# Kernel optimization log

Hardware: AMD Instinct MI355X
Metric: run time of the kernel (lower is better)

The kernel has to match this reference:

```python
import jax, jax.numpy as jnp
import numpy as np

L = 16          # num transformer layers
D = 1024        # d_model
H = 16          # num heads
HD = 64         # head dim
LDIM = 512      # latent dim
TC = 512        # text conditioning length
PAST = 1024     # kv cache past length
FF = 4096       # ffn hidden
FH = 2048       # flow net hidden
MAX_PERIOD = 10000.0


def _ln(x, w, b, eps=1e-5):
    mu = jnp.mean(x, axis=-1, keepdims=True)
    var = jnp.mean((x - mu) ** 2, axis=-1, keepdims=True)
    return (x - mu) * jax.lax.rsqrt(var + eps) * w + b


def setup_inputs() -> dict:
    key = jax.random.key(0)
    ks = jax.random.split(key, 13)
    n = lambda k, s: jax.random.normal(k, s, dtype=jnp.float32)
    inp = {
        'text_embeddings': n(ks[0], (1, TC, D)),
        'prev_latent': n(ks[1], (1, 1, LDIM)),
        'kv_cache': n(ks[2], (L, 2, 1, PAST, H, HD)),
        'cache_len': PAST,
        'noise': n(ks[3], (1, LDIM)),
        'bos_emb': n(ks[4], (LDIM,)),
        'W_in': n(ks[5], (LDIM, D)) * 0.02, 'b_in': jnp.zeros((D,), jnp.float32),
        'ln1_w': jnp.ones((L, D), jnp.float32), 'ln1_b': jnp.zeros((L, D), jnp.float32),
        'Wqkv': n(ks[6], (L, D, 3 * D)) * 0.02, 'bqkv': jnp.zeros((L, 3 * D), jnp.float32),
        'Wo': n(ks[7], (L, D, D)) * 0.02, 'bo': jnp.zeros((L, D), jnp.float32),
        'ln2_w': jnp.ones((L, D), jnp.float32), 'ln2_b': jnp.zeros((L, D), jnp.float32),
        'W1': n(ks[8], (L, D, FF)) * 0.02, 'b1': jnp.zeros((L, FF), jnp.float32),
        'W2': n(ks[9], (L, FF, D)) * 0.02, 'b2': jnp.zeros((L, D), jnp.float32),
        'on_w': jnp.ones((D,), jnp.float32), 'on_b': jnp.zeros((D,), jnp.float32),
        'W_eos': n(ks[10], (D, 1)) * 0.02, 'b_eos': jnp.zeros((1,), jnp.float32),
        'Wf1': n(ks[11], (D + 2 + LDIM, FH)) * 0.02, 'bf1': jnp.zeros((FH,), jnp.float32),
        'Wf2': n(ks[12], (FH, LDIM)) * 0.02, 'bf2': jnp.zeros((LDIM,), jnp.float32),
    }
    return inp


def reference(text_embeddings, prev_latent, kv_cache, cache_len, noise, bos_emb,
              W_in, b_in, ln1_w, ln1_b, Wqkv, bqkv, Wo, bo, ln2_w, ln2_b,
              W1, b1, W2, b2, on_w, on_b, W_eos, b_eos, Wf1, bf1, Wf2, bf2):
    B = prev_latent.shape[0]
    prev = jnp.where(jnp.isnan(prev_latent), bos_emb[None, None, :], prev_latent)
    x = jnp.concatenate([text_embeddings, prev @ W_in + b_in], axis=1)  # [B,T,D]
    T = x.shape[1]
    Tkv = kv_cache.shape[3] + T

    # RoPE angles, shared across layers (offset = cache_len)
    half = HD // 2
    freqs = jnp.exp(jnp.arange(half, dtype=jnp.float32) * (-np.log(MAX_PERIOD) * 2.0 / HD))
    ts = jnp.arange(T, dtype=jnp.float32) + jnp.asarray(cache_len, jnp.float32)
    ang = ts[:, None] * freqs[None, :]               # [T, half]
    cos = jnp.cos(ang)[None, :, None, :]             # [1,T,1,half]
    sin = jnp.sin(ang)[None, :, None, :]

    # causal mask: new token q can see all past + itself
    mask = jnp.arange(Tkv)[None, :] <= (Tkv - T + jnp.arange(T)[:, None])  # [T,Tkv]
    scale = 1.0 / np.sqrt(HD)

    def rot(t):
        tr = t.reshape(B, T, H, half, 2)
        r, i = tr[..., 0], tr[..., 1]
        return jnp.stack([r * cos - i * sin, r * sin + i * cos], axis=-1).reshape(B, T, H, HD)

    def layer_fn(xc, p):
        l1w, l1b, wqkv, bq, wo, bo_, l2w, l2b, w1, b1_, w2, b2_, kv = p
        h = _ln(xc, l1w, l1b)
        qkv = (h @ wqkv + bq).reshape(B, T, 3, H, HD)
        q, k, v = qkv[:, :, 0], qkv[:, :, 1], qkv[:, :, 2]
        q, k = rot(q), rot(k)
        q = q.transpose(0, 2, 1, 3)                  # [B,H,T,HD]
        k = k.transpose(0, 2, 1, 3)
        v = v.transpose(0, 2, 1, 3)
        pk = kv[0].transpose(0, 2, 1, 3)             # [B,H,past,HD]
        pv = kv[1].transpose(0, 2, 1, 3)
        fk = jnp.concatenate([pk, k], axis=2)        # [B,H,Tkv,HD]
        fv = jnp.concatenate([pv, v], axis=2)
        scores = jnp.einsum('bhqd,bhkd->bhqk', q, fk) * scale
        scores = jnp.where(mask[None, None], scores, -1e30)
        attn = jax.nn.softmax(scores, axis=-1)
        o = jnp.einsum('bhqk,bhkd->bhqd', attn, fv).transpose(0, 2, 1, 3).reshape(B, T, D)
        xc = xc + o @ wo + bo_
        h2 = _ln(xc, l2w, l2b)
        xc = xc + jax.nn.gelu(h2 @ w1 + b1_, approximate=False) @ w2 + b2_
        new_kv = jnp.stack([fk.transpose(0, 2, 1, 3), fv.transpose(0, 2, 1, 3)])
        return xc, new_kv

    xs = (ln1_w, ln1_b, Wqkv, bqkv, Wo, bo, ln2_w, ln2_b, W1, b1, W2, b2, kv_cache)
    x, new_kv_cache = jax.lax.scan(layer_fn, x, xs)

    x = _ln(x.astype(jnp.float32), on_w, on_b)
    t_out = x[:, -1, :]                              # [B,D]
    is_eos = (t_out @ W_eos + b_eos) > -4.0
    s_time = jnp.zeros((B, 1), noise.dtype)
    t_time = jnp.ones((B, 1), noise.dtype)
    f_in = jnp.concatenate([t_out, s_time, t_time, noise], axis=-1)
    flow_dir = jax.nn.gelu(f_in @ Wf1 + bf1, approximate=False) @ Wf2 + bf2
    next_latent = noise + flow_dir
    new_cache_len = cache_len + T
    return next_latent, is_eos, new_kv_cache, new_cache_len
```

## Files before the change

kernel.cpp:

```cpp
#include <hip/hip_runtime.h>
#include <math.h>

#define KV_LS_STRIDE 1573888
#define KV_OUT_OFF 513
#define CLEN_OUT_IDX 50364929
#define VTP 1600
#define KVL 1638400

typedef __attribute__((ext_vector_type(8))) short short8;
typedef __attribute__((ext_vector_type(4))) short short4v;
typedef __attribute__((ext_vector_type(4))) float f32x4;

static __device__ __forceinline__ float gelu_f(float v){
  return 0.5f * v * (1.0f + erff(v * 0.70710678118654752f));
}
static __device__ __forceinline__ unsigned short f2b(float f){
  unsigned int u = __float_as_uint(f);
  u += 0x7fffu + ((u>>16)&1u);
  return (unsigned short)(u>>16);
}
__device__ __forceinline__ void gload16(const void* g, void* l){
  __builtin_amdgcn_global_load_lds((const __attribute__((address_space(1))) void*)g,
                                   (__attribute__((address_space(3))) void*)l, 16, 0, 0);
}

__global__ __launch_bounds__(256) void copy_text_k(const float4* __restrict__ t,
                                                   float4* __restrict__ x){
  int i = blockIdx.x*256 + threadIdx.x;
  x[i] = t[i];
}

__global__ __launch_bounds__(256) void build512_k(const float* __restrict__ prev,
    const float* __restrict__ bos, const float* __restrict__ Win,
    const float* __restrict__ bin, float* __restrict__ x){
  __shared__ float red[16][17];
  int t = threadIdx.x;
  int n = blockIdx.x*16 + (t&15), ks = t>>4;
  float s = 0.f;
  for (int k=ks*32; k<ks*32+32; ++k){
    float p = prev[k];
    if (p != p) p = bos[k];
    s += p * Win[(size_t)k*1024 + n];
  }
  red[ks][t&15] = s;
  __syncthreads();
  if (t < 16){
    float acc = bin[blockIdx.x*16 + t];
    #pragma unroll
    for (int j=0;j<16;++j) acc += red[j][t];
    x[(size_t)512*1024 + blockIdx.x*16 + t] = acc;
  }
}

__global__ __launch_bounds__(256) void rope_tab_k(float* __restrict__ cost,
    float* __restrict__ sint, const int* __restrict__ clen){
  int i = blockIdx.x*256 + threadIdx.x;
  if (i >= 513*32) return;
  int t = i >> 5, j = i & 31;
  float freq = expf((float)j * (-0.28782313662425572f));
  float ang = (float)(t + clen[0]) * freq;
  cost[i] = cosf(ang);
  sint[i] = sinf(ang);
}

template<int BF16OUT>
__global__ __launch_bounds__(256) void ln_k(const float* __restrict__ x,
    const float* __restrict__ w, const float* __restrict__ b,
    float* __restrict__ outf, unsigned short* __restrict__ outh, int rows){
  int row = blockIdx.x; if (row >= rows) return;
  const float* xr = x + (size_t)row*1024;
  int tid = threadIdx.x;
  float4 v = *(const float4*)(xr + tid*4);
  float s  = v.x+v.y+v.z+v.w;
  float ss = v.x*v.x+v.y*v.y+v.z*v.z+v.w*v.w;
  for (int o=32;o;o>>=1){ s += __shfl_down(s,o); ss += __shfl_down(ss,o); }
  __shared__ float red[8];
  int wid = tid>>6;
  if ((tid&63)==0){ red[wid]=s; red[4+wid]=ss; }
  __syncthreads();
  if (tid==0){
    float ts = red[0]+red[1]+red[2]+red[3];
    float tss= red[4]+red[5]+red[6]+red[7];
    float mu = ts*(1.0f/1024.0f);
    float var= tss*(1.0f/1024.0f) - mu*mu;
    red[0]=mu; red[1]=rsqrtf(var + 1e-5f);
  }
  __syncthreads();
  float mu = red[0], rs = red[1];
  float4 wv = *(const float4*)(w + tid*4);
  float4 bv = *(const float4*)(b + tid*4);
  float4 o4;
  o4.x = (v.x-mu)*rs*wv.x + bv.x;
  o4.y = (v.y-mu)*rs*wv.y + bv.y;
  o4.z = (v.z-mu)*rs*wv.z + bv.z;
  o4.w = (v.w-mu)*rs*wv.w + bv.w;
  if (BF16OUT){
    uint2 u;
    u.x = (unsigned)f2b(o4.x) | ((unsigned)f2b(o4.y)<<16);
    u.y = (unsigned)f2b(o4.z) | ((unsigned)f2b(o4.w)<<16);
    *(uint2*)(outh + (size_t)row*1024 + tid*4) = u;
  } else {
    *(float4*)(outf + (size_t)row*1024 + tid*4) = o4;
  }
}

__global__ __launch_bounds__(256) void wtrans_k(const float* __restrict__ W,
    unsigned short* __restrict__ Wt, int K, int N){
  __shared__ float s[64][68];
  int l = blockIdx.z;
  W  += (size_t)l*K*N;
  Wt += (size_t)l*N*K;
  int t = threadIdx.x;
  int n0 = blockIdx.x*64, k0 = blockIdx.y*64;
  int r = t>>4, c4 = (t&15)<<2;
  #pragma unroll
  for (int p=0;p<4;++p){
    float4 v = *(const float4*)(W + (size_t)(k0 + r + p*16)*N + n0 + c4);
    *(float4*)&s[r + p*16][c4] = v;
  }
  __syncthreads();
  int n = t>>2, ks = t&3;
  unsigned short tmp[16];
  #pragma unroll
  for (int j=0;j<16;++j) tmp[j] = f2b(s[ks*16 + j][n]);
  size_t ob = (size_t)(n0+n)*K + k0 + ks*16;
  uint4 lo, hi;
  lo.x = tmp[0] | ((unsigned)tmp[1]<<16);  lo.y = tmp[2] | ((unsigned)tmp[3]<<16);
  lo.z = tmp[4] | ((unsigned)tmp[5]<<16);  lo.w = tmp[6] | ((unsigned)tmp[7]<<16);
  hi.x = tmp[8] | ((unsigned)tmp[9]<<16);  hi.y = tmp[10]| ((unsigned)tmp[11]<<16);
  hi.z = tmp[12]| ((unsigned)tmp[13]<<16); hi.w = tmp[14]| ((unsigned)tmp[15]<<16);
  *(uint4*)(Wt + ob)     = lo;
  *(uint4*)(Wt + ob + 8) = hi;
}

template<int MODE>
__global__ __launch_bounds__(256,4) void mgemm64_k(const unsigned short* __restrict__ A,
    const unsigned short* __restrict__ Bt, float* __restrict__ P,
    const float* __restrict__ bias, unsigned short* __restrict__ outh,
    int M, int N, int K, int kc,
    const float* __restrict__ cost, const float* __restrict__ sint,
    unsigned short* __restrict__ qb16, unsigned short* __restrict__ kb16,
    unsigned short* __restrict__ vt, float* __restrict__ kl, float* __restrict__ vl){
  __shared__ unsigned short Alds[2][64*64];
  __shared__ unsigned short Blds[2][64*64];
  int tid = threadIdx.x;
  int w = tid>>6, l = tid&63;
  int m0 = blockIdx.y*64, n0 = blockIdx.x*64;
  int k0 = blockIdx.z*kc, k1 = k0+kc;
  f32x4 acc[2][2];
  #pragma unroll
  for (int i=0;i<2;++i)
    #pragma unroll
    for (int j=0;j<2;++j) acc[i][j] = (f32x4){0.f,0.f,0.f,0.f};
  int srow = l>>3;
  int scol = (((l&7) ^ (srow&7)))*8;
  const unsigned short* ga  = A  + (size_t)(m0 + w*16 + srow)*K + scol;
  const unsigned short* gbp = Bt + (size_t)(n0 + w*16 + srow)*K + scol;
  int lofs = w*16*64;
  int wr = w>>1, wc = w&1, lr = l&15, lg = l>>4;
  int sw = (lr&7)<<3;
  gload16(ga + k0,                &Alds[0][lofs]);
  gload16(ga + (size_t)8*K + k0,  &Alds[0][lofs + 512]);
  gload16(gbp + k0,               &Blds[0][lofs]);
  gload16(gbp + (size_t)8*K + k0, &Blds[0][lofs + 512]);
  __syncthreads();
  int cur = 0;
  for (int k=k0; k<k1; k+=64){
    if (k + 64 < k1){
      int nb = cur^1, kn = k + 64;
      gload16(ga + kn,                &Alds[nb][lofs]);
      gload16(ga + (size_t)8*K + kn,  &Alds[nb][lofs + 512]);
      gload16(gbp + kn,               &Blds[nb][lofs]);
      gload16(gbp + (size_t)8*K + kn, &Blds[nb][lofs + 512]);
    }
    const unsigned short* la = &Alds[cur][0];
    const unsigned short* lb = &Blds[cur][0];
    #pragma unroll
    for (int kk=0; kk<2; ++kk){
      short8 af[2], bfr[2];
      #pragma unroll
      for (int mi=0;mi<2;++mi)
        af[mi] = *(const short8*)&la[(wr*32 + mi*16 + lr)*64 + ((kk*32 + lg*8) ^ sw)];
      #pragma unroll
      for (int ni=0;ni<2;++ni)
        bfr[ni] = *(const short8*)&lb[(wc*32 + ni*16 + lr)*64 + ((kk*32 + lg*8) ^ sw)];
      #pragma unroll
      for (int mi=0;mi<2;++mi)
        #pragma unroll
        for (int ni=0;ni<2;++ni)
          acc[mi][ni] = __builtin_amdgcn_mfma_f32_16x16x32_bf16(af[mi], bfr[ni], acc[mi][ni], 0, 0, 0);
    }
    __syncthreads();
    cur ^= 1;
  }
  if constexpr (MODE==3){
    int nt = n0 >> 6;
    int kind = nt >> 4;
    int hh = nt & 15;
    #pragma unroll
    for (int mi=0;mi<2;++mi){
      int rb = m0 + wr*32 + mi*16 + lg*4;
      #pragma unroll
      for (int ni=0;ni<2;++ni){
        int d = wc*32 + ni*16 + lr;
        float bcol = bias[n0 + d];
        if (kind == 2){
          unsigned short pk[4];
          #pragma unroll
          for (int r=0;r<4;++r){
            float v = acc[mi][ni][r] + bcol;
            pk[r] = f2b(v);
            int t = rb + r;
            if (t < 513) vl[(size_t)(1024+t)*1024 + hh*64 + d] = v;
          }
          uint2 u2;
          u2.x = pk[0] | ((unsigned)pk[1]<<16);
          u2.y = pk[2] | ((unsigned)pk[3]<<16);
          *(uint2*)(vt + (size_t)(hh*64+d)*VTP + 1024 + rb) = u2;
        } else {
          int j = d >> 1;
          #pragma unroll
          for (int r=0;r<4;++r){
            float v = acc[mi][ni][r] + bcol;
            float p = __shfl_xor(v, 1);
            int t = rb + r;
            int tc = (t < 513) ? t : 0;
            float c = cost[(tc<<5)+j], s = sint[(tc<<5)+j];
            float o = (d&1) ? (p*s + v*c) : (v*c - p*s);
            if (t < 513){
              if (kind == 0){
                qb16[(size_t)t*1024 + hh*64 + d] = f2b(o*0.125f);
              } else {
                size_t ko = (size_t)(1024+t)*1024 + hh*64 + d;
                kb16[ko] = f2b(o);
                kl[ko] = o;
              }
            }
          }
        }
      }
    }
  } else {
    float* Pz = P + (size_t)blockIdx.z*M*N;
    #pragma unroll
    for (int mi=0;mi<2;++mi){
      int rb = m0 + wr*32 + mi*16 + lg*4;
      #pragma unroll
      for (int ni=0;ni<2;++ni){
        int col = n0 + wc*32 + ni*16 + lr;
        float bcol = (MODE!=0) ? bias[col] : 0.f;
        #pragma unroll
        for (int r=0;r<4;++r){
          int row = rb + r;
          if (row < M){
            if constexpr (MODE==0){
              Pz[(size_t)row*N + col] = acc[mi][ni][r];
            } else {
              outh[(size_t)row*N + col] = f2b(gelu_f(acc[mi][ni][r] + bcol));
            }
          }
        }
      }
    }
  }
}

template<int KS, int DOLN>
__global__ __launch_bounds__(256) void reduce_ln_k(const float* __restrict__ P,
    const float* __restrict__ bias, float* __restrict__ x,
    const float* __restrict__ lnw, const float* __restrict__ lnb,
    unsigned short* __restrict__ outh){
  const int M = 513;
  int row = blockIdx.x;
  int tid = threadIdx.x;
  int c4 = tid<<2;
  float4 sv = *(const float4*)(P + (size_t)row*1024 + c4);
  #pragma unroll
  for (int z=1; z<KS; ++z){
    float4 t = *(const float4*)(P + (size_t)z*M*1024 + (size_t)row*1024 + c4);
    sv.x+=t.x; sv.y+=t.y; sv.z+=t.z; sv.w+=t.w;
  }
  float4 bv = *(const float4*)(bias + c4);
  float4 xv = *(const float4*)(x + (size_t)row*1024 + c4);
  xv.x += sv.x+bv.x; xv.y += sv.y+bv.y; xv.z += sv.z+bv.z; xv.w += sv.w+bv.w;
  *(float4*)(x + (size_t)row*1024 + c4) = xv;
  if constexpr (DOLN){
    float s  = xv.x+xv.y+xv.z+xv.w;
    float ss = xv.x*xv.x+xv.y*xv.y+xv.z*xv.z+xv.w*xv.w;
    for (int o=32;o;o>>=1){ s += __shfl_down(s,o); ss += __shfl_down(ss,o); }
    __shared__ float red[8];
    int wid = tid>>6;
    if ((tid&63)==0){ red[wid]=s; red[4+wid]=ss; }
    __syncthreads();
    if (tid==0){
      float ts = red[0]+red[1]+red[2]+red[3];
      float tss= red[4]+red[5]+red[6]+red[7];
      float mu = ts*(1.0f/1024.0f);
      float var= tss*(1.0f/1024.0f) - mu*mu;
      red[0]=mu; red[1]=rsqrtf(var + 1e-5f);
    }
    __syncthreads();
    float mu = red[0], rs = red[1];
    float4 wv = *(const float4*)(lnw + c4);
    float4 bb = *(const float4*)(lnb + c4);
    float o0 = (xv.x-mu)*rs*wv.x + bb.x;
    float o1 = (xv.y-mu)*rs*wv.y + bb.y;
    float o2 = (xv.z-mu)*rs*wv.z + bb.z;
    float o3 = (xv.w-mu)*rs*wv.w + bb.w;
    uint2 u;
    u.x = (unsigned)f2b(o0) | ((unsigned)f2b(o1)<<16);
    u.y = (unsigned)f2b(o2) | ((unsigned)f2b(o3)<<16);
    *(uint2*)(outh + (size_t)row*1024 + c4) = u;
  }
}

__global__ __launch_bounds__(256) void past16_k(const float* __restrict__ kvin,
    unsigned short* __restrict__ kb, unsigned short* __restrict__ vt,
    float* __restrict__ kvout){
  __shared__ float s[64][68];
  int l = blockIdx.z;
  int hh = blockIdx.x, t0 = blockIdx.y*64;
  const float* kvK = kvin + (size_t)l*2097152;
  const float* kvV = kvK + 1048576;
  unsigned short* kbL = kb + (size_t)l*KVL;
  unsigned short* vtL = vt + (size_t)l*KVL;
  float* kl = kvout + (size_t)(2*l)  *KV_LS_STRIDE;
  float* vl = kvout + (size_t)(2*l+1)*KV_LS_STRIDE;
  int tid = threadIdx.x;
  int row = tid>>4, c4 = (tid&15)<<2;
  #pragma unroll
  for (int p=0;p<4;++p){
    int rr = row + p*16;
    size_t off = (size_t)(t0+rr)*1024 + hh*64 + c4;
    float4 v = *(const float4*)(kvK + off);
    uint2 u;
    u.x = (unsigned)f2b(v.x) | ((unsigned)f2b(v.y)<<16);
    u.y = (unsigned)f2b(v.z) | ((unsigned)f2b(v.w)<<16);
    *(uint2*)(kbL + off) = u;
    kl[off]=v.x; kl[off+1]=v.y; kl[off+2]=v.z; kl[off+3]=v.w;
    float4 w = *(const float4*)(kvV + off);
    *(float4*)&s[rr][c4] = w;
    vl[off]=w.x; vl[off+1]=w.y; vl[off+2]=w.z; vl[off+3]=w.w;
  }
  __syncthreads();
  int n = tid>>2, ks = tid&3;
  unsigned short tmp[16];
  #pragma unroll
  for (int j=0;j<16;++j) tmp[j] = f2b(s[ks*16+j][n]);
  size_t ob = (size_t)(hh*64+n)*VTP + t0 + ks*16;
  uint4 lo, hi;
  lo.x = tmp[0] | ((unsigned)tmp[1]<<16);  lo.y = tmp[2] | ((unsigned)tmp[3]<<16);
  lo.z = tmp[4] | ((unsigned)tmp[5]<<16);  lo.w = tmp[6] | ((unsigned)tmp[7]<<16);
  hi.x = tmp[8] | ((unsigned)tmp[9]<<16);  hi.y = tmp[10]| ((unsigned)tmp[11]<<16);
  hi.z = tmp[12]| ((unsigned)tmp[13]<<16); hi.w = tmp[14]| ((unsigned)tmp[15]<<16);
  *(uint4*)(vtL + ob)     = lo;
  *(uint4*)(vtL + ob + 8) = hi;
}

static __device__ __forceinline__ f32x4 mfma32(short8 a, short8 b, f32x4 c){
  return __builtin_amdgcn_mfma_f32_16x16x32_bf16(a, b, c, 0, 0, 0);
}

__global__ __launch_bounds__(128) void attn_k(const unsigned short* __restrict__ qb,
    const unsigned short* __restrict__ kb, const unsigned short* __restrict__ vt,
    float* __restrict__ Oc, float* __restrict__ ml){
  const int T=513, Tkv=1537, past=1024;
  int hh = blockIdx.x, bt = blockIdx.y, ch = blockIdx.z;
  int wv = threadIdx.x >> 6, l = threadIdx.x & 63;
  int g = l >> 4, lr = l & 15;
  int q0 = bt*32 + wv*16;
  int gq = q0 + lr;
  const unsigned short* qp = qb + (size_t)gq*1024 + hh*64 + g*8;
  short8 qf0 = *(const short8*)qp;
  short8 qf1 = *(const short8*)(qp+32);
  f32x4 acc_o[4];
  #pragma unroll
  for (int i=0;i<4;++i) acc_o[i] = (f32x4){0.f,0.f,0.f,0.f};
  float m_run = -1e30f, l_run = 0.f;
  int kend_w = past + q0 + 16; if (kend_w > Tkv) kend_w = Tkv;
  int kstart = ch*384;
  int kend = (ch==3) ? kend_w : ((ch+1)*384 < kend_w ? (ch+1)*384 : kend_w);
  for (int kt0 = kstart; kt0 < kend; kt0 += 64){
    float p[16];
    #pragma unroll
    for (int st=0; st<4; ++st){
      const unsigned short* kp = kb + (size_t)(kt0+st*16+lr)*1024 + hh*64 + g*8;
      short8 kf0 = *(const short8*)kp;
      short8 kf1 = *(const short8*)(kp+32);
      f32x4 s4 = (f32x4){0.f,0.f,0.f,0.f};
      s4 = mfma32(kf0, qf0, s4);
      s4 = mfma32(kf1, qf1, s4);
      #pragma unroll
      for (int r=0;r<4;++r) p[st*4+r] = s4[r];
    }
    if (kt0 + 63 > past + q0 + 15 || kt0 + 63 >= Tkv){
      #pragma unroll
      for (int st=0; st<4; ++st)
        #pragma unroll
        for (int r=0;r<4;++r){
          int kt = kt0 + st*16 + g*4 + r;
          if (kt > past + gq || kt >= Tkv) p[st*4+r] = -1e30f;
        }
    }
    float tmax = p[0];
    #pragma unroll
    for (int i=1;i<16;++i) tmax = fmaxf(tmax, p[i]);
    tmax = fmaxf(tmax, __shfl_xor(tmax,16));
    tmax = fmaxf(tmax, __shfl_xor(tmax,32));
    float m_new = fmaxf(m_run, tmax);
    float sc = __expf(m_run - m_new);
    float psum = 0.f;
    #pragma unroll
    for (int i=0;i<16;++i){ p[i] = __expf(p[i] - m_new); psum += p[i]; }
    psum += __shfl_xor(psum,16); psum += __shfl_xor(psum,32);
    l_run = l_run*sc + psum;
    m_run = m_new;
    #pragma unroll
    for (int db=0;db<4;++db){
      acc_o[db][0]*=sc; acc_o[db][1]*=sc; acc_o[db][2]*=sc; acc_o[db][3]*=sc;
    }
    short8 pf[2];
    #pragma unroll
    for (int sp=0; sp<2; ++sp){
      union { short8 s8; unsigned int u[4]; } pu;
      pu.u[0] = (unsigned)f2b(p[sp*8+0]) | ((unsigned)f2b(p[sp*8+1])<<16);
      pu.u[1] = (unsigned)f2b(p[sp*8+2]) | ((unsigned)f2b(p[sp*8+3])<<16);
      pu.u[2] = (unsigned)f2b(p[sp*8+4]) | ((unsigned)f2b(p[sp*8+5])<<16);
      pu.u[3] = (unsigned)f2b(p[sp*8+6]) | ((unsigned)f2b(p[sp*8+7])<<16);
      pf[sp] = pu.s8;
    }
    #pragma unroll
    for (int sp=0; sp<2; ++sp){
      #pragma unroll
      for (int db=0; db<4; ++db){
        const unsigned short* vp = vt + (size_t)(hh*64 + db*16 + lr)*VTP + kt0 + sp*32 + g*4;
        short4v va0 = *(const short4v*)vp;
        short4v va1 = *(const short4v*)(vp + 16);
        short8 va = (short8){va0[0],va0[1],va0[2],va0[3],va1[0],va1[1],va1[2],va1[3]};
        acc_o[db] = mfma32(va, pf[sp], acc_o[db]);
      }
    }
  }
  if (gq < T){
    size_t ob = ((size_t)(ch*16+hh)*544 + gq)*64;
    #pragma unroll
    for (int db=0;db<4;++db)
      *(float4*)(Oc + ob + db*16 + g*4) = make_float4(acc_o[db][0],acc_o[db][1],acc_o[db][2],acc_o[db][3]);
    if (g==0){
      size_t mo = ((size_t)(ch*16+hh)*544 + gq)*2;
      ml[mo] = m_run; ml[mo+1] = l_run;
    }
  }
}

__global__ __launch_bounds__(256) void attn_comb_k(const float* __restrict__ Oc,
    const float* __restrict__ ml, unsigned short* __restrict__ obb){
  int qg = blockIdx.x;
  int t = threadIdx.x;
  int hh = t>>4, d4 = (t&15)<<2;
  float m[4], lv[4];
  float mm = -1e30f;
  #pragma unroll
  for (int c=0;c<4;++c){
    size_t mo = ((size_t)(c*16+hh)*544 + qg)*2;
    m[c]=ml[mo]; lv[c]=ml[mo+1];
    mm = fmaxf(mm, m[c]);
  }
  float w[4], denom = 0.f;
  #pragma unroll
  for (int c=0;c<4;++c){ w[c] = __expf(m[c]-mm); denom += lv[c]*w[c]; }
  float inv = 1.0f/denom;
  float r0=0.f,r1=0.f,r2=0.f,r3=0.f;
  #pragma unroll
  for (int c=0;c<4;++c){
    float4 o = *(const float4*)(Oc + (((size_t)(c*16+hh)*544+qg)*64 + d4));
    r0 += o.x*w[c]; r1 += o.y*w[c]; r2 += o.z*w[c]; r3 += o.w*w[c];
  }
  r0*=inv; r1*=inv; r2*=inv; r3*=inv;
  uint2 u;
  u.x = (unsigned)f2b(r0) | ((unsigned)f2b(r1)<<16);
  u.y = (unsigned)f2b(r2) | ((unsigned)f2b(r3)<<16);
  *(uint2*)(obb + (size_t)qg*1024 + hh*64 + d4) = u;
}

__global__ __launch_bounds__(256) void eos_tail_k(const float* __restrict__ tout,
    const float* __restrict__ Weos, const float* __restrict__ beos,
    const int* __restrict__ clen, float* __restrict__ out){
  int tid = threadIdx.x;
  float s = 0.f;
  for (int i=tid;i<1024;i+=256) s += tout[i]*Weos[i];
  for (int o=32;o;o>>=1) s += __shfl_down(s,o);
  __shared__ float red[4];
  if ((tid&63)==0) red[tid>>6] = s;
  __syncthreads();
  if (tid==0){
    float v = red[0]+red[1]+red[2]+red[3] + beos[0];
    out[512] = (v > -4.0f) ? 1.0f : 0.0f;
    out[CLEN_OUT_IDX] = (float)(clen[0] + 513);
  }
}

__global__ __launch_bounds__(256) void flow1_k(const float* __restrict__ tout,
    const float* __restrict__ noise, const float* __restrict__ Wf1,
    const float* __restrict__ bf1, float* __restrict__ fh){
  __shared__ float red[16][17];
  int t = threadIdx.x;
  int n = blockIdx.x*16 + (t&15), ks = t>>4;
  float s = 0.f;
  for (int k=ks*96; k<ks*96+96; ++k){
    float in = (k < 1024) ? tout[k] : noise[k-1024];
    size_t krow = (k < 1024) ? (size_t)k : (size_t)(k+2);
    s += in * Wf1[krow*2048 + n];
  }
  red[ks][t&15] = s;
  __syncthreads();
  if (t < 16){
    int nn = blockIdx.x*16 + t;
    float acc = bf1[nn] + Wf1[(size_t)1025*2048 + nn];
    #pragma unroll
    for (int j=0;j<16;++j) acc += red[j][t];
    fh[nn] = gelu_f(acc);
  }
}

__global__ __launch_bounds__(256) void flow2_k(const float* __restrict__ fh,
    const float* __restrict__ noise, const float* __restrict__ Wf2,
    const float* __restrict__ bf2, float* __restrict__ out){
  __shared__ float red[16][17];
  int t = threadIdx.x;
  int n = blockIdx.x*16 + (t&15), ks = t>>4;
  float s = 0.f;
  for (int k=ks*128; k<ks*128+128; ++k) s += fh[k]*Wf2[(size_t)k*512 + n];
  red[ks][t&15] = s;
  __syncthreads();
  if (t < 16){
    int nn = blockIdx.x*16 + t;
    float acc = bf2[nn];
    #pragma unroll
    for (int j=0;j<16;++j) acc += red[j][t];
    out[nn] = noise[nn] + acc;
  }
}

extern "C" void kernel_launch(void* const* d_in, const int* in_sizes, int n_in,
                              void* d_out, int out_size, void* d_ws, size_t ws_size,
                              hipStream_t stream) {
  const float* text  = (const float*)d_in[0];
  const float* prevl = (const float*)d_in[1];
  const float* kvin  = (const float*)d_in[2];
  const int*   clen  = (const int*)  d_in[3];
  const float* noise = (const float*)d_in[4];
  const float* bos   = (const float*)d_in[5];
  const float* Win   = (const float*)d_in[6];
  const float* bin   = (const float*)d_in[7];
  const float* ln1w  = (const float*)d_in[8];
  const float* ln1b  = (const float*)d_in[9];
  const float* Wqkv  = (const float*)d_in[10];
  const float* bqkv  = (const float*)d_in[11];
  const float* Wo    = (const float*)d_in[12];
  const float* bo    = (const float*)d_in[13];
  const float* ln2w  = (const float*)d_in[14];
  const float* ln2b  = (const float*)d_in[15];
  const float* W1    = (const float*)d_in[16];
  const float* b1    = (const float*)d_in[17];
  const float* W2    = (const float*)d_in[18];
  const float* b2    = (const float*)d_in[19];
  const float* onw   = (const float*)d_in[20];
  const float* onb   = (const float*)d_in[21];
  const float* Weos  = (const float*)d_in[22];
  const float* beos  = (const float*)d_in[23];
  const float* Wf1   = (const float*)d_in[24];
  const float* bf1   = (const float*)d_in[25];
  const float* Wf2   = (const float*)d_in[26];
  const float* bf2   = (const float*)d_in[27];

  float* out   = (float*)d_out;
  float* kvout = out + KV_OUT_OFF;
  float* ws = (float*)d_ws;
  float* x    = ws;
  float* Pbuf = x    + 525312;
  float* Oc   = Pbuf + 4202496;
  float* mlb  = Oc   + 2228224;
  float* cost = mlb  + 69632;
  float* sint = cost + 16416;
  float* tout = sint + 16416;
  float* fh   = tout + 1024;
  unsigned short* hb   = (unsigned short*)(fh + 2048);
  unsigned short* gb   = hb   + 655360;
  unsigned short* obb  = gb   + 2621440;
  unsigned short* qb16 = obb  + 655360;
  unsigned short* kb16 = qb16 + 557056;
  unsigned short* vt16 = kb16 + (size_t)16*KVL;
  unsigned short* qkvT = vt16 + (size_t)16*KVL;
  unsigned short* woT  = qkvT + (size_t)16*3145728;
  unsigned short* w1T  = woT  + (size_t)16*1048576;
  unsigned short* w2T  = w1T  + (size_t)16*4194304;

  past16_k<<<dim3(16,16,16),256,0,stream>>>(kvin, kb16, vt16, kvout);
  wtrans_k<<<dim3(48,16,16),256,0,stream>>>(Wqkv, qkvT, 1024, 3072);
  wtrans_k<<<dim3(16,16,16),256,0,stream>>>(Wo,   woT,  1024, 1024);
  wtrans_k<<<dim3(64,16,16),256,0,stream>>>(W1,   w1T,  1024, 4096);
  wtrans_k<<<dim3(16,64,16),256,0,stream>>>(W2,   w2T,  4096, 1024);
  copy_text_k<<<512,256,0,stream>>>((const float4*)text, (float4*)x);
  build512_k<<<64,256,0,stream>>>(prevl, bos, Win, bin, x);
  rope_tab_k<<<65,256,0,stream>>>(cost, sint, clen);
  ln_k<1><<<513,256,0,stream>>>(x, ln1w, ln1b, nullptr, hb, 513);

  for (int l=0; l<16; ++l){
    float* kl = kvout + (size_t)(2*l)  *KV_LS_STRIDE;
    float* vl = kvout + (size_t)(2*l+1)*KV_LS_STRIDE;
    unsigned short* kbL = kb16 + (size_t)l*KVL;
    unsigned short* vtL = vt16 + (size_t)l*KVL;
    mgemm64_k<3><<<dim3(48,9),256,0,stream>>>(hb, qkvT+(size_t)l*3145728, nullptr,
        bqkv+(size_t)l*3072, nullptr, 513, 3072, 1024, 1024,
        cost, sint, qb16, kbL, vtL, kl, vl);
    attn_k<<<dim3(16,17,4),128,0,stream>>>(qb16, kbL, vtL, Oc, mlb);
    attn_comb_k<<<513,256,0,stream>>>(Oc, mlb, obb);
    mgemm64_k<0><<<dim3(16,9,4),256,0,stream>>>(obb, woT+(size_t)l*1048576, Pbuf,
        nullptr, nullptr, 513, 1024, 1024, 256,
        nullptr, nullptr, nullptr, nullptr, nullptr, nullptr, nullptr);
    reduce_ln_k<4,1><<<513,256,0,stream>>>(Pbuf, bo+(size_t)l*1024, x,
        ln2w+(size_t)l*1024, ln2b+(size_t)l*1024, hb);
    mgemm64_k<2><<<dim3(64,9),256,0,stream>>>(hb, w1T+(size_t)l*4194304, nullptr,
        b1+(size_t)l*4096, gb, 513, 4096, 1024, 1024,
        nullptr, nullptr, nullptr, nullptr, nullptr, nullptr, nullptr);
    mgemm64_k<0><<<dim3(16,9,4),256,0,stream>>>(gb, w2T+(size_t)l*4194304, Pbuf,
        nullptr, nullptr, 513, 1024, 4096, 1024,
        nullptr, nullptr, nullptr, nullptr, nullptr, nullptr, nullptr);
    if (l < 15)
      reduce_ln_k<4,1><<<513,256,0,stream>>>(Pbuf, b2+(size_t)l*1024, x,
          ln1w+(size_t)(l+1)*1024, ln1b+(size_t)(l+1)*1024, hb);
    else
      reduce_ln_k<4,0><<<513,256,0,stream>>>(Pbuf, b2+(size_t)l*1024, x,
          nullptr, nullptr, nullptr);
  }

  ln_k<0><<<1,256,0,stream>>>(x + (size_t)512*1024, onw, onb, tout, nullptr, 1);
  eos_tail_k<<<1,256,0,stream>>>(tout, Weos, beos, clen, out);
  flow1_k<<<128,256,0,stream>>>(tout, noise, Wf1, bf1, fh);
  flow2_k<<<32,256,0,stream>>>(fh, noise, Wf2, bf2, out);
}
```

Before: 2.312 ms.

## Split K across warps in mgemm64 with LDS reduction instead of output tiling

Each of the four warps now computes the full 64x64 output tile over a separate 32-wide slice of a 128-wide K step, where before each warp owned a 32x32 quadrant. The partial sums are then combined through shared memory in two stages, and only warp 0 runs the epilogue. The K step doubles and the double buffering is removed, so each iteration issues more loads per sync, which is meant to cut barrier and loop overhead. The cost is 64 accumulator registers per lane (launch bounds lowered to 3), a serialized reduction with extra barriers, a single-warp epilogue, no overlap between loads and compute, and an implicit requirement that kc be a multiple of 128.

Result: slower. 2.568 ms (+11.0%).

```diff
diff --git a/kernel.cpp b/kernel.cpp
--- a/kernel.cpp
+++ b/kernel.cpp
@@ -134,75 +134,126 @@
 }
 
 template<int MODE>
-__global__ __launch_bounds__(256,4) void mgemm64_k(const unsigned short* __restrict__ A,
+__global__ __launch_bounds__(256,3) void mgemm64_k(const unsigned short* __restrict__ A,
     const unsigned short* __restrict__ Bt, float* __restrict__ P,
     const float* __restrict__ bias, unsigned short* __restrict__ outh,
     int M, int N, int K, int kc,
     const float* __restrict__ cost, const float* __restrict__ sint,
     unsigned short* __restrict__ qb16, unsigned short* __restrict__ kb16,
     unsigned short* __restrict__ vt, float* __restrict__ kl, float* __restrict__ vl){
-  __shared__ unsigned short Alds[2][64*64];
-  __shared__ unsigned short Blds[2][64*64];
+  __shared__ __align__(16) unsigned short sbuf[16384];
   int tid = threadIdx.x;
   int w = tid>>6, l = tid&63;
   int m0 = blockIdx.y*64, n0 = blockIdx.x*64;
   int k0 = blockIdx.z*kc, k1 = k0+kc;
-  f32x4 acc[2][2];
-  #pragma unroll
-  for (int i=0;i<2;++i)
-    #pragma unroll
-    for (int j=0;j<2;++j) acc[i][j] = (f32x4){0.f,0.f,0.f,0.f};
-  int srow = l>>3;
-  int scol = (((l&7) ^ (srow&7)))*8;
-  const unsigned short* ga  = A  + (size_t)(m0 + w*16 + srow)*K + scol;
-  const unsigned short* gbp = Bt + (size_t)(n0 + w*16 + srow)*K + scol;
-  int lofs = w*16*64;
-  int wr = w>>1, wc = w&1, lr = l&15, lg = l>>4;
-  int sw = (lr&7)<<3;
-  gload16(ga + k0,                &Alds[0][lofs]);
-  gload16(ga + (size_t)8*K + k0,  &Alds[0][lofs + 512]);
-  gload16(gbp + k0,               &Blds[0][lofs]);
-  gload16(gbp + (size_t)8*K + k0, &Blds[0][lofs + 512]);
-  __syncthreads();
-  int cur = 0;
-  for (int k=k0; k<k1; k+=64){
-    if (k + 64 < k1){
-      int nb = cur^1, kn = k + 64;
-      gload16(ga + kn,                &Alds[nb][lofs]);
-      gload16(ga + (size_t)8*K + kn,  &Alds[nb][lofs + 512]);
-      gload16(gbp + kn,               &Blds[nb][lofs]);
-      gload16(gbp + (size_t)8*K + kn, &Blds[nb][lofs + 512]);
-    }
-    const unsigned short* la = &Alds[cur][0];
-    const unsigned short* lb = &Blds[cur][0];
-    #pragma unroll
-    for (int kk=0; kk<2; ++kk){
-      short8 af[2], bfr[2];
-      #pragma unroll
-      for (int mi=0;mi<2;++mi)
-        af[mi] = *(const short8*)&la[(wr*32 + mi*16 + lr)*64 + ((kk*32 + lg*8) ^ sw)];
-      #pragma unroll
-      for (int ni=0;ni<2;++ni)
-        bfr[ni] = *(const short8*)&lb[(wc*32 + ni*16 + lr)*64 + ((kk*32 + lg*8) ^ sw)];
-      #pragma unroll
-      for (int mi=0;mi<2;++mi)
+  f32x4 acc[4][4];
+  #pragma unroll
+  for (int i=0;i<4;++i)
+    #pragma unroll
+    for (int j=0;j<4;++j) acc[i][j] = (f32x4){0.f,0.f,0.f,0.f};
+  int lrow = l>>4, lc = l&15;
+  int halfc = lc>>3, qc = lc&7;
+  const unsigned short* gA[4]; const unsigned short* gB[4];
+  unsigned short* lA[4]; unsigned short* lB[4];
+  #pragma unroll
+  for (int p=0;p<4;++p){
+    int ch = w*4 + p;
+    int rA = ch*4 + lrow;
+    int colg = halfc*64 + ((qc ^ (rA&7))<<3);
+    gA[p] = A  + (size_t)(m0 + rA)*K + colg;
+    gB[p] = Bt + (size_t)(n0 + rA)*K + colg;
+    lA[p] = &sbuf[ch*512];
+    lB[p] = &sbuf[8192 + ch*512];
+  }
+  int lr = l&15, lg = l>>4;
+  int colr = ((w>>1)<<6) + ((((w&1)<<5) + (lg<<3)) ^ ((lr&7)<<3));
+  for (int k=k0; k<k1; k+=128){
+    #pragma unroll
+    for (int p=0;p<4;++p) gload16(gA[p] + k, lA[p]);
+    #pragma unroll
+    for (int p=0;p<4;++p) gload16(gB[p] + k, lB[p]);
+    __syncthreads();
+    short8 af[4], bfr[4];
+    #pragma unroll
+    for (int mi=0;mi<4;++mi)
+      af[mi] = *(const short8*)&sbuf[(mi*16+lr)*128 + colr];
+    #pragma unroll
+    for (int ni=0;ni<4;++ni)
+      bfr[ni] = *(const short8*)&sbuf[8192 + (ni*16+lr)*128 + colr];
+    #pragma unroll
+    for (int mi=0;mi<4;++mi)
+      #pragma unroll
+      for (int ni=0;ni<4;++ni)
+        acc[mi][ni] = __builtin_amdgcn_mfma_f32_16x16x32_bf16(af[mi], bfr[ni], acc[mi][ni], 0, 0, 0);
+    __syncthreads();
+  }
+  float* redA = (float*)sbuf;
+  float* redB = (float*)(sbuf + 8192);
+  if (w == 2){
+    #pragma unroll
+    for (int mi=0;mi<4;++mi)
+      #pragma unroll
+      for (int ni=0;ni<4;++ni)
         #pragma unroll
-        for (int ni=0;ni<2;++ni)
-          acc[mi][ni] = __builtin_amdgcn_mfma_f32_16x16x32_bf16(af[mi], bfr[ni], acc[mi][ni], 0, 0, 0);
-    }
-    __syncthreads();
-    cur ^= 1;
-  }
+        for (int r=0;r<4;++r)
+          redA[(mi*16+lg*4+r)*64 + ni*16+lr] = acc[mi][ni][r];
+  } else if (w == 3){
+    #pragma unroll
+    for (int mi=0;mi<4;++mi)
+      #pragma unroll
+      for (int ni=0;ni<4;++ni)
+        #pragma unroll
+        for (int r=0;r<4;++r)
+          redB[(mi*16+lg*4+r)*64 + ni*16+lr] = acc[mi][ni][r];
+  }
+  __syncthreads();
+  if (w == 0){
+    #pragma unroll
+    for (int mi=0;mi<4;++mi)
+      #pragma unroll
+      for (int ni=0;ni<4;++ni)
+        #pragma unroll
+        for (int r=0;r<4;++r)
+          acc[mi][ni][r] += redA[(mi*16+lg*4+r)*64 + ni*16+lr];
+  } else if (w == 1){
+    #pragma unroll
+    for (int mi=0;mi<4;++mi)
+      #pragma unroll
+      for (int ni=0;ni<4;++ni)
+        #pragma unroll
+        for (int r=0;r<4;++r)
+          acc[mi][ni][r] += redB[(mi*16+lg*4+r)*64 + ni*16+lr];
+  }
+  __syncthreads();
+  if (w == 1){
+    #pragma unroll
+    for (int mi=0;mi<4;++mi)
+      #pragma unroll
+      for (int ni=0;ni<4;++ni)
+        #pragma unroll
+        for (int r=0;r<4;++r)
+          redA[(mi*16+lg*4+r)*64 + ni*16+lr] = acc[mi][ni][r];
+  }
+  __syncthreads();
+  if (w != 0) return;
+  #pragma unroll
+  for (int mi=0;mi<4;++mi)
+    #pragma unroll
+    for (int ni=0;ni<4;++ni)
+      #pragma unroll
+      for (int r=0;r<4;++r)
+        acc[mi][ni][r] += redA[(mi*16+lg*4+r)*64 + ni*16+lr];
+
   if constexpr (MODE==3){
     int nt = n0 >> 6;
     int kind = nt >> 4;
     int hh = nt & 15;
     #pragma unroll
-    for (int mi=0;mi<2;++mi){
-      int rb = m0 + wr*32 + mi*16 + lg*4;
-      #pragma unroll
-      for (int ni=0;ni<2;++ni){
-        int d = wc*32 + ni*16 + lr;
+    for (int mi=0;mi<4;++mi){
+      int rb = m0 + mi*16 + lg*4;
+      #pragma unroll
+      for (int ni=0;ni<4;++ni){
+        int d = ni*16 + lr;
         float bcol = bias[n0 + d];
         if (kind == 2){
           unsigned short pk[4];
@@ -243,11 +294,11 @@
   } else {
     float* Pz = P + (size_t)blockIdx.z*M*N;
     #pragma unroll
-    for (int mi=0;mi<2;++mi){
-      int rb = m0 + wr*32 + mi*16 + lg*4;
-      #pragma unroll
-      for (int ni=0;ni<2;++ni){
-        int col = n0 + wc*32 + ni*16 + lr;
+    for (int mi=0;mi<4;++mi){
+      int rb = m0 + mi*16 + lg*4;
+      #pragma unroll
+      for (int ni=0;ni<4;++ni){
+        int col = n0 + ni*16 + lr;
         float bcol = (MODE!=0) ? bias[col] : 0.f;
         #pragma unroll
         for (int r=0;r<4;++r){
```
